# Optimization experiments

Measured on AMD Instinct MI355X. Metric: run time of the kernel, lower is better.

The kernel has to match this reference:

```python
import jax, jax.numpy as jnp
import numpy as np

GROUP_SIZE = 7      # init: group_size
SAMPLING_RATIO = 2  # init: sampling_ratio


def setup_inputs() -> dict:
    key = jax.random.key(0)
    k_feat, k_b, k_x, k_y, k_w, k_h = jax.random.split(key, 6)
    B, C, H, W = 2, 490, 160, 160          # C = output_dim(10) * group_size^2(49)
    stride = 16
    img = stride * H                        # 2560 px image space
    N = 512
    features = jax.random.normal(k_feat, (B, C, H, W), dtype=jnp.float32)
    b_idx = jax.random.randint(k_b, (N,), 0, B).astype(jnp.float32)
    x1 = jax.random.uniform(k_x, (N,)) * (img * 0.6)
    y1 = jax.random.uniform(k_y, (N,)) * (img * 0.6)
    w = 16.0 + jax.random.uniform(k_w, (N,)) * (img * 0.35)
    h = 16.0 + jax.random.uniform(k_h, (N,)) * (img * 0.35)
    rois = jnp.stack([b_idx, x1, y1, x1 + w, y1 + h], axis=1).astype(jnp.float32)
    return {"rois": rois, "features": features, "stride": stride}


def _axis_indices(coord, size):
    """Per-axis bilinear indices/fraction with RoIAlign boundary handling.
    coord: [...]; returns low, high (int32), frac, valid mask."""
    valid = (coord > -1.0) & (coord < size)
    c = jnp.maximum(coord, 0.0)
    low = jnp.floor(c).astype(jnp.int32)
    low = jnp.minimum(low, size - 1)
    high = jnp.minimum(low + 1, size - 1)
    frac = jnp.where(low >= size - 1, 0.0, c - low.astype(coord.dtype))
    return low, high, frac, valid


def _psroi_align(rois, features, stride, g, sr):
    spatial_scale = 1.0 / stride
    B, C, H, W = features.shape
    D = C // (g * g)  # output_dim
    # position-sensitive channel map: c = (ctop*g + ph)*g + pw -> [D, g, g]
    ch = (jnp.arange(D)[:, None, None] * g + jnp.arange(g)[None, :, None]) * g \
         + jnp.arange(g)[None, None, :]

    def per_roi(roi):
        b = roi[0].astype(jnp.int32)
        sw = roi[1] * spatial_scale - 0.5
        sh = roi[2] * spatial_scale - 0.5
        ew = roi[3] * spatial_scale - 0.5
        eh = roi[4] * spatial_scale - 0.5
        roi_w = jnp.maximum(ew - sw, 0.1)
        roi_h = jnp.maximum(eh - sh, 0.1)
        bin_h = roi_h / g
        bin_w = roi_w / g
        # sample grid: [g, sr] coordinates along each axis
        off = (jnp.arange(sr, dtype=jnp.float32) + 0.5) / sr
        ys = sh + (jnp.arange(g, dtype=jnp.float32)[:, None] + off[None, :]) * bin_h
        xs = sw + (jnp.arange(g, dtype=jnp.float32)[:, None] + off[None, :]) * bin_w
        ylo, yhi, ly, vy = _axis_indices(ys, H)  # [g, sr]
        xlo, xhi, lx, vx = _axis_indices(xs, W)  # [g, sr]
        hy, hx = 1.0 - ly, 1.0 - lx
        feat = features[b]  # [C, H, W]

        def gather(yi, xi):
            # -> [D, g, g, sr, sr]
            return feat[ch[:, :, :, None, None],
                        yi[None, :, None, :, None],
                        xi[None, None, :, None, :]]

        wy = lambda a: a[None, :, None, :, None]
        wx = lambda a: a[None, None, :, None, :]
        val = (wy(hy) * wx(hx) * gather(ylo, xlo)
               + wy(hy) * wx(lx) * gather(ylo, xhi)
               + wy(ly) * wx(hx) * gather(yhi, xlo)
               + wy(ly) * wx(lx) * gather(yhi, xhi))
        mask = vy[None, :, None, :, None] & vx[None, None, :, None, :]
        val = jnp.where(mask, val, 0.0)
        return val.mean(axis=(3, 4))  # average over sr*sr samples -> [D, g, g]

    return jax.vmap(per_roi)(rois[:, :5])


def reference(rois, features, stride):
    return _psroi_align(rois, features, stride, GROUP_SIZE, SAMPLING_RATIO)
```

## Files before the change

### kernel.cpp

```cpp
#include <hip/hip_runtime.h>
#include <hip/hip_bf16.h>


#define G 7
#define SR 2
#define D_OUT 10

__global__ void psroi_align_kernel(const float* __restrict__ rois,
                                   const float* __restrict__ feat,
                                   const int* __restrict__ stride_p,
                                   int N, int B, int C, int H, int W,
                                   float* __restrict__ out) {
    int idx = blockIdx.x * blockDim.x + threadIdx.x;
    int total = N * D_OUT * G * G * (SR * SR);
    if (idx >= total) return;

    int s       = idx & 3;
    int out_idx = idx >> 2;
    int iy = s >> 1;
    int ix = s & 1;

    int iv = stride_p[0];
    float stride_f;
    if (iv > 0 && iv <= 65536) stride_f = (float)iv;
    else                       stride_f = __int_as_float(iv);
    float spatial_scale = 1.0f / stride_f;

    int pw = out_idx % G;
    int ph = (out_idx / G) % G;
    int d  = (out_idx / (G * G)) % D_OUT;
    int n  = out_idx / (G * G * D_OUT);

    const float* roi = rois + (size_t)n * 5;
    int   b  = (int)roi[0];
    float sw = roi[1] * spatial_scale - 0.5f;
    float sh = roi[2] * spatial_scale - 0.5f;
    float ew = roi[3] * spatial_scale - 0.5f;
    float eh = roi[4] * spatial_scale - 0.5f;
    float roi_w = fmaxf(ew - sw, 0.1f);
    float roi_h = fmaxf(eh - sh, 0.1f);
    float bin_h = roi_h / (float)G;
    float bin_w = roi_w / (float)G;

    int c = (d * G + ph) * G + pw;
    const float* __restrict__ fplane = feat + ((size_t)b * C + c) * (size_t)(H * W);

    float y  = sh + ((float)ph + ((float)iy + 0.5f) / (float)SR) * bin_h;
    float x  = sw + ((float)pw + ((float)ix + 0.5f) / (float)SR) * bin_w;
    bool  vy = (y > -1.0f) && (y < (float)H);
    bool  vx = (x > -1.0f) && (x < (float)W);

    float cy = fmaxf(y, 0.0f);
    int  ylo = min((int)floorf(cy), H - 1);
    int  yhi = min(ylo + 1, H - 1);
    float ly = (ylo >= H - 1) ? 0.0f : (cy - (float)ylo);
    float hy = 1.0f - ly;

    float cx = fmaxf(x, 0.0f);
    int  xlo = min((int)floorf(cx), W - 1);
    int  xhi = min(xlo + 1, W - 1);
    float lx = (xlo >= W - 1) ? 0.0f : (cx - (float)xlo);
    float hx = 1.0f - lx;

    float val = 0.0f;
    if (vy && vx) {
        float v00 = fplane[(size_t)ylo * W + xlo];
        float v01 = fplane[(size_t)ylo * W + xhi];
        float v10 = fplane[(size_t)yhi * W + xlo];
        float v11 = fplane[(size_t)yhi * W + xhi];
        val = hy * hx * v00 + hy * lx * v01 + ly * hx * v10 + ly * lx * v11;
    }

    val += __shfl_xor(val, 1);
    val += __shfl_xor(val, 2);
    if (s == 0) out[out_idx] = val * (1.0f / (float)(SR * SR));
}

extern "C" void kernel_launch(void* const* d_in, const int* in_sizes, int n_in,
                              void* d_out, int out_size, void* d_ws, size_t ws_size,
                              hipStream_t stream) {
    const float* rois = (const float*)d_in[0];
    const float* feat = (const float*)d_in[1];
    const int*   strd = (const int*)d_in[2];
    float* out = (float*)d_out;

    int N = in_sizes[0] / 5;
    const int C = D_OUT * G * G;
    const int H = 160, W = 160;
    int B = in_sizes[1] / (C * H * W);

    int total = N * D_OUT * G * G * (SR * SR);
    int block = 256;
    int grid = (total + block - 1) / block;
    psroi_align_kernel<<<grid, block, 0, stream>>>(rois, feat, strd, N, B, C, H, W, out);
}
```

Baseline: 22.70 us.

## Precompute per-ROI sample tables and gather bilinear pairs with 2-wide loads

Splits the work into two kernels. The first precomputes per-ROI x/y sample indices and validity-masked bilinear weights into workspace tables. The second reads these tables and fetches each row's two horizontal neighbours with a single unaligned 2-float load, handling the right-edge clamp by shifting the base index and remapping the weights. This removes redundant per-thread coordinate math and halves the gather load count, in exchange for an extra kernel launch and the table traffic through global memory.

```diff
diff --git a/kernel.cpp b/kernel.cpp
--- a/kernel.cpp
+++ b/kernel.cpp
@@ -5,75 +5,108 @@
 #define G 7
 #define SR 2
 #define D_OUT 10
+#define HH 160
+#define WW 160
 
-__global__ void psroi_align_kernel(const float* __restrict__ rois,
-                                   const float* __restrict__ feat,
-                                   const int* __restrict__ stride_p,
-                                   int N, int B, int C, int H, int W,
-                                   float* __restrict__ out) {
-    int idx = blockIdx.x * blockDim.x + threadIdx.x;
-    int total = N * D_OUT * G * G * (SR * SR);
-    if (idx >= total) return;
+typedef float f2_u __attribute__((ext_vector_type(2), aligned(4)));
 
-    int s       = idx & 3;
-    int out_idx = idx >> 2;
-    int iy = s >> 1;
-    int ix = s & 1;
+__global__ __launch_bounds__(512) void psroi_tables_kernel(
+        const float* __restrict__ rois,
+        const int* __restrict__ stride_p,
+        int N,
+        float4* __restrict__ xtab, float4* __restrict__ ytab,
+        int* __restrict__ btab) {
+    int tid = blockIdx.x * 512 + threadIdx.x;
+    int total = N * G * SR;
+    if (tid >= total) return;
+
+    int j   = tid % SR;
+    int p   = (tid / SR) % G;
+    int n   = tid / (SR * G);
 
     int iv = stride_p[0];
-    float stride_f;
-    if (iv > 0 && iv <= 65536) stride_f = (float)iv;
-    else                       stride_f = __int_as_float(iv);
+    float stride_f = (iv > 0 && iv <= 65536) ? (float)iv : __int_as_float(iv);
     float spatial_scale = 1.0f / stride_f;
 
-    int pw = out_idx % G;
-    int ph = (out_idx / G) % G;
-    int d  = (out_idx / (G * G)) % D_OUT;
-    int n  = out_idx / (G * G * D_OUT);
-
     const float* roi = rois + (size_t)n * 5;
-    int   b  = (int)roi[0];
     float sw = roi[1] * spatial_scale - 0.5f;
     float sh = roi[2] * spatial_scale - 0.5f;
     float ew = roi[3] * spatial_scale - 0.5f;
     float eh = roi[4] * spatial_scale - 0.5f;
-    float roi_w = fmaxf(ew - sw, 0.1f);
-    float roi_h = fmaxf(eh - sh, 0.1f);
-    float bin_h = roi_h / (float)G;
-    float bin_w = roi_w / (float)G;
+    float bh = fmaxf(eh - sh, 0.1f) * (1.0f / (float)G);
+    float bw = fmaxf(ew - sw, 0.1f) * (1.0f / (float)G);
+    float off = (j ? 0.75f : 0.25f);
 
-    int c = (d * G + ph) * G + pw;
-    const float* __restrict__ fplane = feat + ((size_t)b * C + c) * (size_t)(H * W);
+    {
+        float x  = sw + ((float)p + off) * bw;
+        bool  vx = (x > -1.0f) && (x < (float)WW);
+        float cx = fmaxf(x, 0.0f);
+        int  xlo = min((int)floorf(cx), WW - 1);
+        float lx = (xlo >= WW - 1) ? 0.0f : (cx - (float)xlo);
+        float hx = 1.0f - lx;
+        int xbase = min(xlo, WW - 2);
+        bool clamped = (xlo != xbase);
+        float wx0 = (vx && !clamped) ? hx : 0.0f;
+        float wx1 = vx ? (clamped ? hx : lx) : 0.0f;
+        xtab[tid] = make_float4((float)xbase, wx0, wx1, 0.0f);
+    }
+    {
+        float y  = sh + ((float)p + off) * bh;
+        bool  vy = (y > -1.0f) && (y < (float)HH);
+        float cy = fmaxf(y, 0.0f);
+        int  ylo = min((int)floorf(cy), HH - 1);
+        int  yhi = min(ylo + 1, HH - 1);
+        float ly = (ylo >= HH - 1) ? 0.0f : (cy - (float)ylo);
+        float hy = 1.0f - ly;
+        float wy0 = vy ? hy : 0.0f;
+        float wy1 = vy ? ly : 0.0f;
+        ytab[tid] = make_float4((float)ylo, (float)yhi, wy0, wy1);
+    }
+    if (p == 0 && j == 0) btab[n] = (int)roi[0];
+}
 
-    float y  = sh + ((float)ph + ((float)iy + 0.5f) / (float)SR) * bin_h;
-    float x  = sw + ((float)pw + ((float)ix + 0.5f) / (float)SR) * bin_w;
-    bool  vy = (y > -1.0f) && (y < (float)H);
-    bool  vx = (x > -1.0f) && (x < (float)W);
+__global__ __launch_bounds__(256) void psroi_gather_kernel(
+        const float* __restrict__ feat,
+        const float4* __restrict__ xtab, const float4* __restrict__ ytab,
+        const int* __restrict__ btab,
+        int N, int C,
+        float* __restrict__ out) {
+    int idx = blockIdx.x * 256 + threadIdx.x;
+    int total = N * D_OUT * G * G * 4;
+    if (idx >= total) return;
 
-    float cy = fmaxf(y, 0.0f);
-    int  ylo = min((int)floorf(cy), H - 1);
-    int  yhi = min(ylo + 1, H - 1);
-    float ly = (ylo >= H - 1) ? 0.0f : (cy - (float)ylo);
-    float hy = 1.0f - ly;
+    int s  = idx & 3;
+    int o  = idx >> 2;
+    int ix = s & 1;
+    int iy = s >> 1;
 
-    float cx = fmaxf(x, 0.0f);
-    int  xlo = min((int)floorf(cx), W - 1);
-    int  xhi = min(xlo + 1, W - 1);
-    float lx = (xlo >= W - 1) ? 0.0f : (cx - (float)xlo);
-    float hx = 1.0f - lx;
+    int c49 = o % 49;
+    int nd  = o / 49;
+    int ph  = c49 / 7;
+    int pw  = c49 - ph * 7;
+    int n   = nd / D_OUT;
+    int d   = nd - n * D_OUT;
 
-    float val = 0.0f;
-    if (vy && vx) {
-        float v00 = fplane[(size_t)ylo * W + xlo];
-        float v01 = fplane[(size_t)ylo * W + xhi];
-        float v10 = fplane[(size_t)yhi * W + xlo];
-        float v11 = fplane[(size_t)yhi * W + xhi];
-        val = hy * hx * v00 + hy * lx * v01 + ly * hx * v10 + ly * lx * v11;
-    }
+    float4 xt = xtab[(n * G + pw) * SR + ix];
+    float4 yt = ytab[(n * G + ph) * SR + iy];
+    int b = btab[n];
+
+    int c = d * 49 + c49;
+    const float* __restrict__ plane = feat + ((size_t)b * C + c) * (size_t)(HH * WW);
+
+    int xbase = (int)xt.x;
+    int ylo   = (int)yt.x;
+    int yhi   = (int)yt.y;
+
+    f2_u p0 = *(const f2_u*)(plane + ylo * WW + xbase);
+    f2_u p1 = *(const f2_u*)(plane + yhi * WW + xbase);
+
+    float val = yt.z * (xt.y * p0.x + xt.z * p0.y)
+              + yt.w * (xt.y * p1.x + xt.z * p1.y);
 
     val += __shfl_xor(val, 1);
     val += __shfl_xor(val, 2);
-    if (s == 0) out[out_idx] = val * (1.0f / (float)(SR * SR));
+    if (s == 0) out[o] = val * 0.25f;
 }
 
 extern "C" void kernel_launch(void* const* d_in, const int* in_sizes, int n_in,
@@ -86,11 +119,16 @@
 
     int N = in_sizes[0] / 5;
     const int C = D_OUT * G * G;
-    const int H = 160, W = 160;
-    int B = in_sizes[1] / (C * H * W);
 
-    int total = N * D_OUT * G * G * (SR * SR);
-    int block = 256;
-    int grid = (total + block - 1) / block;
-    psroi_align_kernel<<<grid, block, 0, stream>>>(rois, feat, strd, N, B, C, H, W, out);
+    int ntab = N * G * SR;
+    float4* xtab = (float4*)d_ws;
+    float4* ytab = xtab + ntab;
+    int*    btab = (int*)(ytab + ntab);
+
+    int gridA = (ntab + 511) / 512;
+    psroi_tables_kernel<<<gridA, 512, 0, stream>>>(rois, strd, N, xtab, ytab, btab);
+
+    int total = N * D_OUT * G * G * 4;
+    int gridB = (total + 255) / 256;
+    psroi_gather_kernel<<<gridB, 256, 0, stream>>>(feat, xtab, ytab, btab, N, C, out);
 }
```

Measured after the change: 27.86 us. 1.23x slower.
